# Kernel optimization log

Hardware: AMD Instinct MI355X
Metric: run time of the kernel (lower is better)

The kernel has to match this reference:

```python
import jax, jax.numpy as jnp
import numpy as np

N = 50000      # nodes
E = 1_600_000  # edges per relation
D = 128        # input feature dim
H = 64         # gnn_hidden_channel
R = 3          # hetero relations
NEG_SLOPE = 0.2


def setup_inputs() -> dict:
    key = jax.random.key(0)
    ks = jax.random.split(key, 9)
    x = jax.random.normal(ks[0], (N, D), jnp.float32)
    edge_index = jax.random.randint(ks[1], (R, 2, E), 0, N, dtype=jnp.int32)
    edge_weight = jax.random.uniform(ks[2], (R, E), jnp.float32)
    W0 = jax.random.normal(ks[3], (R, D, H), jnp.float32) / np.float32(np.sqrt(D))
    W1 = jax.random.normal(ks[4], (R, H, H), jnp.float32) / np.float32(np.sqrt(H))
    W2 = jax.random.normal(ks[5], (R, H, H), jnp.float32) / np.float32(np.sqrt(H))
    a_src = jax.random.normal(ks[6], (R, 3, H), jnp.float32) * 0.1
    a_dst = jax.random.normal(ks[7], (R, 3, H), jnp.float32) * 0.1
    bias = jnp.zeros((R, 3, H), jnp.float32)
    return {"x": x, "edge_weight": edge_weight, "W0": W0, "W1": W1, "W2": W2,
            "a_src": a_src, "a_dst": a_dst, "bias": bias, "edge_index": edge_index}


def gat_layer(x, src, dst, ew, W, a_s, a_d, b):
    # GATConv, heads=1: h = xW; e = LeakyReLU(a_s.h_src + a_d.h_dst); softmax over dst
    h = x @ W                                  # [N, H]
    alpha_s = h @ a_s                          # [N]
    alpha_d = h @ a_d                          # [N]
    e = jax.nn.leaky_relu(alpha_s[src] + alpha_d[dst], NEG_SLOPE)  # [Etot]
    m = jax.ops.segment_max(e, dst, num_segments=N)                # per-dst max
    e = jnp.exp(e - m[dst])
    s = jax.ops.segment_sum(e, dst, num_segments=N)
    alpha = (e / (s[dst] + 1e-16)) * ew        # edge_weight scales attention
    out = jax.ops.segment_sum(alpha[:, None] * h[src], dst, num_segments=N)
    return out + b


def reference(x, edge_weight, W0, W1, W2, a_src, a_dst, bias, edge_index):
    loop = jnp.arange(N, dtype=edge_index.dtype)   # self-loops (PyG default)
    ones_w = jnp.ones((N,), x.dtype)
    outs = []
    for r in range(R):
        src = jnp.concatenate([edge_index[r, 0], loop])
        dst = jnp.concatenate([edge_index[r, 1], loop])
        ew = jnp.concatenate([edge_weight[r], ones_w])
        Ws = (W0[r], W1[r], W2[r])
        h = x
        for i in range(3):
            h = gat_layer(h, src, dst, ew, Ws[i], a_src[r, i], a_dst[r, i], bias[r, i])
            if i != 2:
                h = jax.nn.relu(h)
        outs.append(h)
    return jnp.concatenate(outs, axis=1)  # [N, R*H] = [N, 192]
```

## Files before the change

kernel.cpp:

```cpp
#include <hip/hip_runtime.h>
#include <math.h>

#define N_NODES 50000
#define E_EDGES 1600000
#define D_IN 128
#define H_DIM 64
#define R_REL 3
#define ETOT (E_EDGES + N_NODES)
#define NEG_SLOPE 0.2f

#define BSHIFT 8
#define BSIZE 256
#define NBUCK ((N_NODES + BSIZE - 1) / BSIZE)
#define CHUNK 4096
#define NBLK ((ETOT + CHUNK - 1) / CHUNK)

template <int DIN>
__global__ __launch_bounds__(256) void gemm_alpha_kernel(
    const float* __restrict__ xin,
    const float* __restrict__ W,
    const float* __restrict__ a_s,
    const float* __restrict__ a_d,
    float* __restrict__ h,
    float* __restrict__ as_out,
    float* __restrict__ ad_out)
{
    constexpr int KC = 64;
    constexpr int XSTR = KC + 4;
    __shared__ __align__(16) float xls[64 * XSTR];
    __shared__ __align__(16) float wls[KC * 64];
    int t = threadIdx.x;
    int n0 = blockIdx.x * 64;
    int nrows = N_NODES - n0; if (nrows > 64) nrows = 64;
    int tn = t >> 4;
    int tc = t & 15;

    float4 acc[4] = {{0,0,0,0},{0,0,0,0},{0,0,0,0},{0,0,0,0}};

    for (int kc = 0; kc < DIN; kc += KC) {
        if (kc) __syncthreads();
        int nf4 = nrows * (KC / 4);
        for (int f = t; f < nf4; f += 256) {
            int row = f >> 4;
            int q = f & 15;
            float4 xv = *reinterpret_cast<const float4*>(
                xin + (size_t)(n0 + row) * DIN + kc + q * 4);
            *reinterpret_cast<float4*>(&xls[row * XSTR + q * 4]) = xv;
        }
        for (int f = t; f < KC * 16; f += 256) {
            int kk = f >> 4;
            int q = f & 15;
            *reinterpret_cast<float4*>(&wls[kk * 64 + q * 4]) =
                *reinterpret_cast<const float4*>(W + (size_t)(kc + kk) * 64 + q * 4);
        }
        __syncthreads();

#pragma unroll
        for (int k4 = 0; k4 < KC / 4; ++k4) {
            float4 av[4], bv[4];
#pragma unroll
            for (int i = 0; i < 4; ++i)
                av[i] = *reinterpret_cast<const float4*>(
                    &xls[(tn * 4 + i) * XSTR + k4 * 4]);
#pragma unroll
            for (int u = 0; u < 4; ++u)
                bv[u] = *reinterpret_cast<const float4*>(
                    &wls[(k4 * 4 + u) * 64 + tc * 4]);
#pragma unroll
            for (int i = 0; i < 4; ++i) {
                acc[i].x = fmaf(av[i].x, bv[0].x, acc[i].x);
                acc[i].y = fmaf(av[i].x, bv[0].y, acc[i].y);
                acc[i].z = fmaf(av[i].x, bv[0].z, acc[i].z);
                acc[i].w = fmaf(av[i].x, bv[0].w, acc[i].w);
                acc[i].x = fmaf(av[i].y, bv[1].x, acc[i].x);
                acc[i].y = fmaf(av[i].y, bv[1].y, acc[i].y);
                acc[i].z = fmaf(av[i].y, bv[1].z, acc[i].z);
                acc[i].w = fmaf(av[i].y, bv[1].w, acc[i].w);
                acc[i].x = fmaf(av[i].z, bv[2].x, acc[i].x);
                acc[i].y = fmaf(av[i].z, bv[2].y, acc[i].y);
                acc[i].z = fmaf(av[i].z, bv[2].z, acc[i].z);
                acc[i].w = fmaf(av[i].z, bv[2].w, acc[i].w);
                acc[i].x = fmaf(av[i].w, bv[3].x, acc[i].x);
                acc[i].y = fmaf(av[i].w, bv[3].y, acc[i].y);
                acc[i].z = fmaf(av[i].w, bv[3].z, acc[i].z);
                acc[i].w = fmaf(av[i].w, bv[3].w, acc[i].w);
            }
        }
    }

    float4 asj = *reinterpret_cast<const float4*>(a_s + tc * 4);
    float4 adj = *reinterpret_cast<const float4*>(a_d + tc * 4);
#pragma unroll
    for (int i = 0; i < 4; ++i) {
        int node = n0 + tn * 4 + i;
        bool ok = node < N_NODES;
        if (ok)
            *reinterpret_cast<float4*>(h + (size_t)node * 64 + tc * 4) = acc[i];
        float vs = acc[i].x * asj.x + acc[i].y * asj.y +
                   acc[i].z * asj.z + acc[i].w * asj.w;
        float vd = acc[i].x * adj.x + acc[i].y * adj.y +
                   acc[i].z * adj.z + acc[i].w * adj.w;
#pragma unroll
        for (int m = 8; m >= 1; m >>= 1) {
            vs += __shfl_xor(vs, m, 64);
            vd += __shfl_xor(vd, m, 64);
        }
        if (ok && tc == 0) {
            as_out[node] = vs;
            ad_out[node] = vd;
        }
    }
}

__global__ __launch_bounds__(256) void partA_hist(const int* __restrict__ dstE,
                                                  int* __restrict__ bh)
{
    __shared__ int hist[NBUCK];
    int t = threadIdx.x, blk = blockIdx.x;
    for (int b = t; b < NBUCK; b += 256) hist[b] = 0;
    __syncthreads();
    int base = blk * CHUNK;
#pragma unroll
    for (int u = 0; u < CHUNK / 256; ++u) {
        int i = base + u * 256 + t;
        if (i < ETOT) {
            int d = (i < E_EDGES) ? dstE[i] : (i - E_EDGES);
            atomicAdd(&hist[d >> BSHIFT], 1);
        }
    }
    __syncthreads();
    for (int b = t; b < NBUCK; b += 256) bh[(size_t)blk * NBUCK + b] = hist[b];
}

__global__ __launch_bounds__(256) void partA2_scan(int* __restrict__ bh,
                                                   int* __restrict__ btot)
{
    __shared__ int tmp[256];
    __shared__ int carry_s;
    int b = blockIdx.x, t = threadIdx.x;
    if (t == 0) carry_s = 0;
    __syncthreads();
    for (int base = 0; base < NBLK; base += 256) {
        int idx = base + t;
        int v = (idx < NBLK) ? bh[(size_t)idx * NBUCK + b] : 0;
        int x = v;
#pragma unroll
        for (int off = 1; off < 256; off <<= 1) {
            tmp[t] = x;
            __syncthreads();
            int a = (t >= off) ? tmp[t - off] : 0;
            __syncthreads();
            x += a;
        }
        int carry = carry_s;
        if (idx < NBLK) bh[(size_t)idx * NBUCK + b] = carry + x - v;
        __syncthreads();
        if (t == 255) carry_s = carry + x;
        __syncthreads();
    }
    if (t == 0) btot[b] = carry_s;
}

__global__ __launch_bounds__(256) void partA3_scan(const int* __restrict__ btot,
                                                   int* __restrict__ bbase)
{
    __shared__ int tmp[256];
    int t = threadIdx.x;
    int v = (t < NBUCK) ? btot[t] : 0;
    int x = v;
#pragma unroll
    for (int off = 1; off < 256; off <<= 1) {
        tmp[t] = x;
        __syncthreads();
        int a = (t >= off) ? tmp[t - off] : 0;
        __syncthreads();
        x += a;
    }
    if (t < NBUCK) bbase[t] = x - v;
    if (t == 255) bbase[NBUCK] = x;
}

__global__ __launch_bounds__(256) void partB_scatter(
    const int* __restrict__ srcE, const int* __restrict__ dstE,
    const float* __restrict__ ewr, const int* __restrict__ bh,
    const int* __restrict__ bbase, int2* __restrict__ psw)
{
    __shared__ int cur[NBUCK];
    int t = threadIdx.x, blk = blockIdx.x;
    for (int b = t; b < NBUCK; b += 256)
        cur[b] = bbase[b] + bh[(size_t)blk * NBUCK + b];
    __syncthreads();
    int base = blk * CHUNK;
#pragma unroll
    for (int u = 0; u < CHUNK / 256; ++u) {
        int i = base + u * 256 + t;
        if (i < ETOT) {
            int s, d;
            float w;
            if (i < E_EDGES) {
                s = srcE[i]; d = dstE[i]; w = ewr[i];
            } else {
                s = d = i - E_EDGES; w = 1.0f;
            }
            int pos = atomicAdd(&cur[d >> BSHIFT], 1);
            int2 pay;
            pay.x = s | ((d & (BSIZE - 1)) << 16);
            pay.y = __float_as_int(w);
            psw[pos] = pay;
        }
    }
}

__global__ __launch_bounds__(256) void partC_sort(
    const int* __restrict__ bbase, const int2* __restrict__ psw,
    int* __restrict__ rs, int2* __restrict__ sedge)
{
    __shared__ int cnt[BSIZE];
    __shared__ int rsl[BSIZE];
    __shared__ int tmp[BSIZE];
    __shared__ int cur[BSIZE];
    int b = blockIdx.x, t = threadIdx.x;
    int lo = b * BSIZE;
    int nn = N_NODES - lo; if (nn > BSIZE) nn = BSIZE;
    int seg0 = bbase[b], seg1 = bbase[b + 1];
    cnt[t] = 0; cur[t] = 0;
    __syncthreads();
    for (int k = seg0 + t; k < seg1; k += 256)
        atomicAdd(&cnt[(psw[k].x >> 16) & 255], 1);
    __syncthreads();
    int v = cnt[t], x = v;
#pragma unroll
    for (int off = 1; off < 256; off <<= 1) {
        tmp[t] = x;
        __syncthreads();
        int a = (t >= off) ? tmp[t - off] : 0;
        __syncthreads();
        x += a;
    }
    rsl[t] = x - v;
    __syncthreads();
    if (t < nn) rs[lo + t] = seg0 + rsl[t];
    if (b == NBUCK - 1 && t == 0) rs[N_NODES] = seg1;
    for (int k = seg0 + t; k < seg1; k += 256) {
        int2 pw = psw[k];
        int dlo = (pw.x >> 16) & 255;
        int pos = seg0 + rsl[dlo] + atomicAdd(&cur[dlo], 1);
        int2 rec;
        rec.x = pw.x & 0xFFFF;
        rec.y = pw.y;
        sedge[pos] = rec;
    }
}

__global__ __launch_bounds__(256) void agg_kernel(
    const int* __restrict__ rs, const int2* __restrict__ sedge,
    const float* __restrict__ as_v, const float* __restrict__ ad_v,
    const float* __restrict__ h,
    const float* __restrict__ bias,
    float* __restrict__ out, int out_stride, int do_relu)
{
    int wave = (int)(((size_t)blockIdx.x * blockDim.x + threadIdx.x) >> 6);
    int lane = threadIdx.x & 63;
    if (wave >= N_NODES) return;
    int beg = rs[wave], end = rs[wave + 1];
    float ad_n = ad_v[wave];

    int sub = lane >> 4;
    int f = lane & 15;
    const float* hf = h + f * 4;

    float ssum = 0.f;
    float4 a0 = {0.f, 0.f, 0.f, 0.f};
    float4 a1 = a0, a2 = a0, a3 = a0;

    for (int cbeg = beg; cbeg < end; cbeg += 64) {
        int rem = end - cbeg;
        int srcv = 0;
        float pq = 0.f;
        if (lane < rem) {
            int2 pe = sedge[cbeg + lane];
            srcv = pe.x;
            float e = as_v[srcv] + ad_n;
            e = (e > 0.f) ? e : NEG_SLOPE * e;
            float p = __expf(e);
            ssum += p;
            pq = p * __int_as_float(pe.y);
        }
        for (int t0 = 0; t0 < rem; t0 += 16) {
            int s0 = __shfl(srcv, t0 + sub, 64);
            float q0 = __shfl(pq, t0 + sub, 64);
            int s1 = __shfl(srcv, t0 + 4 + sub, 64);
            float q1 = __shfl(pq, t0 + 4 + sub, 64);
            int s2 = __shfl(srcv, t0 + 8 + sub, 64);
            float q2 = __shfl(pq, t0 + 8 + sub, 64);
            int s3 = __shfl(srcv, t0 + 12 + sub, 64);
            float q3 = __shfl(pq, t0 + 12 + sub, 64);
            float4 h0 = *reinterpret_cast<const float4*>(hf + (size_t)s0 * 64);
            float4 h1 = *reinterpret_cast<const float4*>(hf + (size_t)s1 * 64);
            float4 h2 = *reinterpret_cast<const float4*>(hf + (size_t)s2 * 64);
            float4 h3 = *reinterpret_cast<const float4*>(hf + (size_t)s3 * 64);
            a0.x = fmaf(q0, h0.x, a0.x);
            a0.y = fmaf(q0, h0.y, a0.y);
            a0.z = fmaf(q0, h0.z, a0.z);
            a0.w = fmaf(q0, h0.w, a0.w);
            a1.x = fmaf(q1, h1.x, a1.x);
            a1.y = fmaf(q1, h1.y, a1.y);
            a1.z = fmaf(q1, h1.z, a1.z);
            a1.w = fmaf(q1, h1.w, a1.w);
            a2.x = fmaf(q2, h2.x, a2.x);
            a2.y = fmaf(q2, h2.y, a2.y);
            a2.z = fmaf(q2, h2.z, a2.z);
            a2.w = fmaf(q2, h2.w, a2.w);
            a3.x = fmaf(q3, h3.x, a3.x);
            a3.y = fmaf(q3, h3.y, a3.y);
            a3.z = fmaf(q3, h3.z, a3.z);
            a3.w = fmaf(q3, h3.w, a3.w);
        }
    }

    float4 acc;
    acc.x = (a0.x + a1.x) + (a2.x + a3.x);
    acc.y = (a0.y + a1.y) + (a2.y + a3.y);
    acc.z = (a0.z + a1.z) + (a2.z + a3.z);
    acc.w = (a0.w + a1.w) + (a2.w + a3.w);

#pragma unroll
    for (int off = 32; off > 0; off >>= 1) ssum += __shfl_xor(ssum, off, 64);
    acc.x += __shfl_xor(acc.x, 16, 64);
    acc.y += __shfl_xor(acc.y, 16, 64);
    acc.z += __shfl_xor(acc.z, 16, 64);
    acc.w += __shfl_xor(acc.w, 16, 64);
    acc.x += __shfl_xor(acc.x, 32, 64);
    acc.y += __shfl_xor(acc.y, 32, 64);
    acc.z += __shfl_xor(acc.z, 32, 64);
    acc.w += __shfl_xor(acc.w, 32, 64);

    if (sub == 0) {
        float inv = 1.f / (ssum + 1e-16f);
        const float4 bv = *reinterpret_cast<const float4*>(bias + f * 4);
        float4 o;
        o.x = fmaf(acc.x, inv, bv.x);
        o.y = fmaf(acc.y, inv, bv.y);
        o.z = fmaf(acc.z, inv, bv.z);
        o.w = fmaf(acc.w, inv, bv.w);
        if (do_relu) {
            o.x = fmaxf(o.x, 0.f);
            o.y = fmaxf(o.y, 0.f);
            o.z = fmaxf(o.z, 0.f);
            o.w = fmaxf(o.w, 0.f);
        }
        *reinterpret_cast<float4*>(out + (size_t)wave * out_stride + f * 4) = o;
    }
}

extern "C" void kernel_launch(void* const* d_in, const int* in_sizes, int n_in,
                              void* d_out, int out_size, void* d_ws, size_t ws_size,
                              hipStream_t stream)
{
    (void)in_sizes; (void)n_in; (void)out_size; (void)ws_size;
    const float* x = (const float*)d_in[0];
    const float* edge_weight = (const float*)d_in[1];
    const float* W0 = (const float*)d_in[2];
    const float* W1 = (const float*)d_in[3];
    const float* W2 = (const float*)d_in[4];
    const float* a_src = (const float*)d_in[5];
    const float* a_dst = (const float*)d_in[6];
    const float* bias = (const float*)d_in[7];
    const int* edge_index = (const int*)d_in[8];
    float* out = (float*)d_out;

    char* ws = (char*)d_ws;
    size_t off = 0;
    auto alloc = [&](size_t bytes) {
        void* p = ws + off;
        off += (bytes + 255) & ~(size_t)255;
        return p;
    };
    int2* sedge = (int2*)alloc((size_t)ETOT * 8);
    int2* psw = (int2*)alloc((size_t)ETOT * 8);
    int* bh = (int*)alloc((size_t)NBLK * NBUCK * 4);
    int* btot = (int*)alloc((size_t)NBUCK * 4);
    int* bbase = (int*)alloc((size_t)(NBUCK + 1) * 4);
    int* rs = (int*)alloc((size_t)(N_NODES + 1) * 4);
    float* hbuf = (float*)alloc((size_t)N_NODES * 64 * 4);
    float* xbuf = (float*)alloc((size_t)N_NODES * 64 * 4);
    float* asv = (float*)alloc((size_t)N_NODES * 4);
    float* adv = (float*)alloc((size_t)N_NODES * 4);

    const int WAVE_BLOCKS = (N_NODES * 64 + 255) / 256;
    const int GEMM_BLOCKS = (N_NODES + 63) / 64;

    for (int r = 0; r < R_REL; ++r) {
        const int* srcE = edge_index + (size_t)r * 2 * E_EDGES;
        const int* dstE = srcE + E_EDGES;
        const float* ewr = edge_weight + (size_t)r * E_EDGES;

        partA_hist<<<NBLK, 256, 0, stream>>>(dstE, bh);
        partA2_scan<<<NBUCK, 256, 0, stream>>>(bh, btot);
        partA3_scan<<<1, 256, 0, stream>>>(btot, bbase);
        partB_scatter<<<NBLK, 256, 0, stream>>>(srcE, dstE, ewr, bh, bbase, psw);
        partC_sort<<<NBUCK, 256, 0, stream>>>(bbase, psw, rs, sedge);

        for (int i = 0; i < 3; ++i) {
            const float* Wl = (i == 0) ? (W0 + (size_t)r * D_IN * H_DIM)
                            : (i == 1) ? (W1 + (size_t)r * H_DIM * H_DIM)
                                       : (W2 + (size_t)r * H_DIM * H_DIM);
            const float* asr = a_src + ((size_t)r * 3 + i) * H_DIM;
            const float* adr = a_dst + ((size_t)r * 3 + i) * H_DIM;
            const float* br = bias + ((size_t)r * 3 + i) * H_DIM;

            if (i == 0)
                gemm_alpha_kernel<D_IN><<<GEMM_BLOCKS, 256, 0, stream>>>(
                    x, Wl, asr, adr, hbuf, asv, adv);
            else
                gemm_alpha_kernel<H_DIM><<<GEMM_BLOCKS, 256, 0, stream>>>(
                    xbuf, Wl, asr, adr, hbuf, asv, adv);

            if (i < 2)
                agg_kernel<<<WAVE_BLOCKS, 256, 0, stream>>>(
                    rs, sedge, asv, adv, hbuf, br, xbuf, 64, 1);
            else
                agg_kernel<<<WAVE_BLOCKS, 256, 0, stream>>>(
                    rs, sedge, asv, adv, hbuf, br, out + r * 64, 192, 0);
        }
    }
}
```

Before: 856.2 us.

## Batch CSR build across relations, sort buckets in place, pipeline aggregation gathers

The histogram, scan, scatter and bucket-sort kernels now run once for all three relations, with the relation index taken from the block index. This cuts launch count and gives each launch a larger grid. Buckets shrink to 128 nodes and chunks grow to 8192 edges, so the block-level scan becomes a single pass. The bucket sort stages each bucket in LDS and writes back in place, which removes the psw buffer. The aggregation loop now prefetches the next group of neighbour rows before doing the FMAs on the current group, and clamps each chunk to 64 lanes. The in-place sort falls back to global reads for buckets larger than CCAP, which would race with its own writes if a bucket ever overflowed.

```diff
diff --git a/kernel.cpp b/kernel.cpp
--- a/kernel.cpp
+++ b/kernel.cpp
@@ -9,11 +9,12 @@
 #define ETOT (E_EDGES + N_NODES)
 #define NEG_SLOPE 0.2f
 
-#define BSHIFT 8
-#define BSIZE 256
+#define BSHIFT 7
+#define BSIZE 128
 #define NBUCK ((N_NODES + BSIZE - 1) / BSIZE)
-#define CHUNK 4096
+#define CHUNK 8192
 #define NBLK ((ETOT + CHUNK - 1) / CHUNK)
+#define CCAP 5120
 
 template <int DIN>
 __global__ __launch_bounds__(256) void gemm_alpha_kernel(
@@ -112,15 +113,18 @@
     }
 }
 
-__global__ __launch_bounds__(256) void partA_hist(const int* __restrict__ dstE,
+__global__ __launch_bounds__(256) void partA_hist(const int* __restrict__ edge_index,
                                                   int* __restrict__ bh)
 {
     __shared__ int hist[NBUCK];
-    int t = threadIdx.x, blk = blockIdx.x;
+    int t = threadIdx.x;
+    int r = blockIdx.x / NBLK;
+    int blk = blockIdx.x % NBLK;
+    const int* dstE = edge_index + (size_t)r * 2 * E_EDGES + E_EDGES;
     for (int b = t; b < NBUCK; b += 256) hist[b] = 0;
     __syncthreads();
     int base = blk * CHUNK;
-#pragma unroll
+#pragma unroll 4
     for (int u = 0; u < CHUNK / 256; ++u) {
         int i = base + u * 256 + t;
         if (i < ETOT) {
@@ -129,20 +133,46 @@
         }
     }
     __syncthreads();
-    for (int b = t; b < NBUCK; b += 256) bh[(size_t)blk * NBUCK + b] = hist[b];
+    int* bh_r = bh + (size_t)r * NBLK * NBUCK;
+    for (int b = t; b < NBUCK; b += 256) bh_r[(size_t)blk * NBUCK + b] = hist[b];
 }
 
 __global__ __launch_bounds__(256) void partA2_scan(int* __restrict__ bh,
                                                    int* __restrict__ btot)
 {
     __shared__ int tmp[256];
+    int r = blockIdx.x / NBUCK;
+    int b = blockIdx.x % NBUCK;
+    int t = threadIdx.x;
+    int* bh_r = bh + (size_t)r * NBLK * NBUCK;
+    int v = (t < NBLK) ? bh_r[(size_t)t * NBUCK + b] : 0;
+    int x = v;
+#pragma unroll
+    for (int off = 1; off < 256; off <<= 1) {
+        tmp[t] = x;
+        __syncthreads();
+        int a = (t >= off) ? tmp[t - off] : 0;
+        __syncthreads();
+        x += a;
+    }
+    if (t < NBLK) bh_r[(size_t)t * NBUCK + b] = x - v;
+    if (t == 255) btot[r * NBUCK + b] = x;
+}
+
+__global__ __launch_bounds__(256) void partA3_scan(const int* __restrict__ btot,
+                                                   int* __restrict__ bbase)
+{
+    __shared__ int tmp[256];
     __shared__ int carry_s;
-    int b = blockIdx.x, t = threadIdx.x;
+    int r = blockIdx.x;
+    int t = threadIdx.x;
+    const int* row = btot + r * NBUCK;
+    int* outb = bbase + r * (NBUCK + 1);
     if (t == 0) carry_s = 0;
     __syncthreads();
-    for (int base = 0; base < NBLK; base += 256) {
+    for (int base = 0; base < NBUCK; base += 256) {
         int idx = base + t;
-        int v = (idx < NBLK) ? bh[(size_t)idx * NBUCK + b] : 0;
+        int v = (idx < NBUCK) ? row[idx] : 0;
         int x = v;
 #pragma unroll
         for (int off = 1; off < 256; off <<= 1) {
@@ -153,45 +183,34 @@
             x += a;
         }
         int carry = carry_s;
-        if (idx < NBLK) bh[(size_t)idx * NBUCK + b] = carry + x - v;
+        if (idx < NBUCK) outb[idx] = carry + x - v;
         __syncthreads();
         if (t == 255) carry_s = carry + x;
         __syncthreads();
     }
-    if (t == 0) btot[b] = carry_s;
-}
-
-__global__ __launch_bounds__(256) void partA3_scan(const int* __restrict__ btot,
-                                                   int* __restrict__ bbase)
-{
-    __shared__ int tmp[256];
-    int t = threadIdx.x;
-    int v = (t < NBUCK) ? btot[t] : 0;
-    int x = v;
-#pragma unroll
-    for (int off = 1; off < 256; off <<= 1) {
-        tmp[t] = x;
-        __syncthreads();
-        int a = (t >= off) ? tmp[t - off] : 0;
-        __syncthreads();
-        x += a;
-    }
-    if (t < NBUCK) bbase[t] = x - v;
-    if (t == 255) bbase[NBUCK] = x;
+    if (t == 0) outb[NBUCK] = carry_s;
 }
 
 __global__ __launch_bounds__(256) void partB_scatter(
-    const int* __restrict__ srcE, const int* __restrict__ dstE,
-    const float* __restrict__ ewr, const int* __restrict__ bh,
-    const int* __restrict__ bbase, int2* __restrict__ psw)
+    const int* __restrict__ edge_index, const float* __restrict__ edge_weight,
+    const int* __restrict__ bh, const int* __restrict__ bbase,
+    int2* __restrict__ sedge)
 {
     __shared__ int cur[NBUCK];
-    int t = threadIdx.x, blk = blockIdx.x;
+    int t = threadIdx.x;
+    int r = blockIdx.x / NBLK;
+    int blk = blockIdx.x % NBLK;
+    const int* srcE = edge_index + (size_t)r * 2 * E_EDGES;
+    const int* dstE = srcE + E_EDGES;
+    const float* ewr = edge_weight + (size_t)r * E_EDGES;
+    const int* bh_r = bh + (size_t)r * NBLK * NBUCK;
+    const int* bbase_r = bbase + r * (NBUCK + 1);
+    int2* se_r = sedge + (size_t)r * ETOT;
     for (int b = t; b < NBUCK; b += 256)
-        cur[b] = bbase[b] + bh[(size_t)blk * NBUCK + b];
+        cur[b] = bbase_r[b] + bh_r[(size_t)blk * NBUCK + b];
     __syncthreads();
     int base = blk * CHUNK;
-#pragma unroll
+#pragma unroll 4
     for (int u = 0; u < CHUNK / 256; ++u) {
         int i = base + u * 256 + t;
         if (i < ETOT) {
@@ -206,49 +225,60 @@
             int2 pay;
             pay.x = s | ((d & (BSIZE - 1)) << 16);
             pay.y = __float_as_int(w);
-            psw[pos] = pay;
+            se_r[pos] = pay;
         }
     }
 }
 
 __global__ __launch_bounds__(256) void partC_sort(
-    const int* __restrict__ bbase, const int2* __restrict__ psw,
-    int* __restrict__ rs, int2* __restrict__ sedge)
-{
+    const int* __restrict__ bbase, int2* __restrict__ sedge,
+    int* __restrict__ rs)
+{
+    __shared__ int2 stage[CCAP];
     __shared__ int cnt[BSIZE];
     __shared__ int rsl[BSIZE];
     __shared__ int tmp[BSIZE];
     __shared__ int cur[BSIZE];
-    int b = blockIdx.x, t = threadIdx.x;
+    int r = blockIdx.x / NBUCK;
+    int b = blockIdx.x % NBUCK;
+    int t = threadIdx.x;
+    const int* bbase_r = bbase + r * (NBUCK + 1);
+    int* rs_r = rs + r * (N_NODES + 1);
+    int2* se_r = sedge + (size_t)r * ETOT;
     int lo = b * BSIZE;
     int nn = N_NODES - lo; if (nn > BSIZE) nn = BSIZE;
-    int seg0 = bbase[b], seg1 = bbase[b + 1];
-    cnt[t] = 0; cur[t] = 0;
-    __syncthreads();
-    for (int k = seg0 + t; k < seg1; k += 256)
-        atomicAdd(&cnt[(psw[k].x >> 16) & 255], 1);
-    __syncthreads();
-    int v = cnt[t], x = v;
-#pragma unroll
-    for (int off = 1; off < 256; off <<= 1) {
-        tmp[t] = x;
-        __syncthreads();
-        int a = (t >= off) ? tmp[t - off] : 0;
+    int seg0 = bbase_r[b], seg1 = bbase_r[b + 1];
+    int len = seg1 - seg0;
+    if (t < BSIZE) { cnt[t] = 0; cur[t] = 0; }
+    __syncthreads();
+    for (int k = t; k < len; k += 256) {
+        int2 pw = se_r[seg0 + k];
+        if (k < CCAP) stage[k] = pw;
+        atomicAdd(&cnt[(pw.x >> 16) & (BSIZE - 1)], 1);
+    }
+    __syncthreads();
+    int v = 0, x = 0;
+    if (t < BSIZE) { v = cnt[t]; x = v; }
+#pragma unroll
+    for (int off = 1; off < BSIZE; off <<= 1) {
+        if (t < BSIZE) tmp[t] = x;
+        __syncthreads();
+        int a = (t < BSIZE && t >= off) ? tmp[t - off] : 0;
         __syncthreads();
         x += a;
     }
-    rsl[t] = x - v;
-    __syncthreads();
-    if (t < nn) rs[lo + t] = seg0 + rsl[t];
-    if (b == NBUCK - 1 && t == 0) rs[N_NODES] = seg1;
-    for (int k = seg0 + t; k < seg1; k += 256) {
-        int2 pw = psw[k];
-        int dlo = (pw.x >> 16) & 255;
-        int pos = seg0 + rsl[dlo] + atomicAdd(&cur[dlo], 1);
+    if (t < BSIZE) rsl[t] = x - v;
+    __syncthreads();
+    if (t < nn) rs_r[lo + t] = seg0 + rsl[t];
+    if (b == NBUCK - 1 && t == 0) rs_r[N_NODES] = seg1;
+    for (int k = t; k < len; k += 256) {
+        int2 pw = (k < CCAP) ? stage[k] : se_r[seg0 + k];
+        int dlo = (pw.x >> 16) & (BSIZE - 1);
+        int pos = rsl[dlo] + atomicAdd(&cur[dlo], 1);
         int2 rec;
         rec.x = pw.x & 0xFFFF;
         rec.y = pw.y;
-        sedge[pos] = rec;
+        se_r[seg0 + pos] = rec;
     }
 }
 
@@ -275,6 +305,7 @@
 
     for (int cbeg = beg; cbeg < end; cbeg += 64) {
         int rem = end - cbeg;
+        if (rem > 64) rem = 64;
         int srcv = 0;
         float pq = 0.f;
         if (lane < rem) {
@@ -286,19 +317,31 @@
             ssum += p;
             pq = p * __int_as_float(pe.y);
         }
-        for (int t0 = 0; t0 < rem; t0 += 16) {
-            int s0 = __shfl(srcv, t0 + sub, 64);
-            float q0 = __shfl(pq, t0 + sub, 64);
-            int s1 = __shfl(srcv, t0 + 4 + sub, 64);
-            float q1 = __shfl(pq, t0 + 4 + sub, 64);
-            int s2 = __shfl(srcv, t0 + 8 + sub, 64);
-            float q2 = __shfl(pq, t0 + 8 + sub, 64);
-            int s3 = __shfl(srcv, t0 + 12 + sub, 64);
-            float q3 = __shfl(pq, t0 + 12 + sub, 64);
-            float4 h0 = *reinterpret_cast<const float4*>(hf + (size_t)s0 * 64);
-            float4 h1 = *reinterpret_cast<const float4*>(hf + (size_t)s1 * 64);
-            float4 h2 = *reinterpret_cast<const float4*>(hf + (size_t)s2 * 64);
-            float4 h3 = *reinterpret_cast<const float4*>(hf + (size_t)s3 * 64);
+        int s0 = __shfl(srcv, sub, 64);
+        float q0 = __shfl(pq, sub, 64);
+        int s1 = __shfl(srcv, 4 + sub, 64);
+        float q1 = __shfl(pq, 4 + sub, 64);
+        int s2 = __shfl(srcv, 8 + sub, 64);
+        float q2 = __shfl(pq, 8 + sub, 64);
+        int s3 = __shfl(srcv, 12 + sub, 64);
+        float q3 = __shfl(pq, 12 + sub, 64);
+        float4 h0 = *reinterpret_cast<const float4*>(hf + (size_t)s0 * 64);
+        float4 h1 = *reinterpret_cast<const float4*>(hf + (size_t)s1 * 64);
+        float4 h2 = *reinterpret_cast<const float4*>(hf + (size_t)s2 * 64);
+        float4 h3 = *reinterpret_cast<const float4*>(hf + (size_t)s3 * 64);
+        for (int t0 = 16; t0 < rem; t0 += 16) {
+            int ns0 = __shfl(srcv, t0 + sub, 64);
+            float nq0 = __shfl(pq, t0 + sub, 64);
+            int ns1 = __shfl(srcv, t0 + 4 + sub, 64);
+            float nq1 = __shfl(pq, t0 + 4 + sub, 64);
+            int ns2 = __shfl(srcv, t0 + 8 + sub, 64);
+            float nq2 = __shfl(pq, t0 + 8 + sub, 64);
+            int ns3 = __shfl(srcv, t0 + 12 + sub, 64);
+            float nq3 = __shfl(pq, t0 + 12 + sub, 64);
+            float4 nh0 = *reinterpret_cast<const float4*>(hf + (size_t)ns0 * 64);
+            float4 nh1 = *reinterpret_cast<const float4*>(hf + (size_t)ns1 * 64);
+            float4 nh2 = *reinterpret_cast<const float4*>(hf + (size_t)ns2 * 64);
+            float4 nh3 = *reinterpret_cast<const float4*>(hf + (size_t)ns3 * 64);
             a0.x = fmaf(q0, h0.x, a0.x);
             a0.y = fmaf(q0, h0.y, a0.y);
             a0.z = fmaf(q0, h0.z, a0.z);
@@ -315,7 +358,27 @@
             a3.y = fmaf(q3, h3.y, a3.y);
             a3.z = fmaf(q3, h3.z, a3.z);
             a3.w = fmaf(q3, h3.w, a3.w);
-        }
+            q0 = nq0; h0 = nh0;
+            q1 = nq1; h1 = nh1;
+            q2 = nq2; h2 = nh2;
+            q3 = nq3; h3 = nh3;
+        }
+        a0.x = fmaf(q0, h0.x, a0.x);
+        a0.y = fmaf(q0, h0.y, a0.y);
+        a0.z = fmaf(q0, h0.z, a0.z);
+        a0.w = fmaf(q0, h0.w, a0.w);
+        a1.x = fmaf(q1, h1.x, a1.x);
+        a1.y = fmaf(q1, h1.y, a1.y);
+        a1.z = fmaf(q1, h1.z, a1.z);
+        a1.w = fmaf(q1, h1.w, a1.w);
+        a2.x = fmaf(q2, h2.x, a2.x);
+        a2.y = fmaf(q2, h2.y, a2.y);
+        a2.z = fmaf(q2, h2.z, a2.z);
+        a2.w = fmaf(q2, h2.w, a2.w);
+        a3.x = fmaf(q3, h3.x, a3.x);
+        a3.y = fmaf(q3, h3.y, a3.y);
+        a3.z = fmaf(q3, h3.z, a3.z);
+        a3.w = fmaf(q3, h3.w, a3.w);
     }
 
     float4 acc;
@@ -376,12 +439,11 @@
         off += (bytes + 255) & ~(size_t)255;
         return p;
     };
-    int2* sedge = (int2*)alloc((size_t)ETOT * 8);
-    int2* psw = (int2*)alloc((size_t)ETOT * 8);
-    int* bh = (int*)alloc((size_t)NBLK * NBUCK * 4);
-    int* btot = (int*)alloc((size_t)NBUCK * 4);
-    int* bbase = (int*)alloc((size_t)(NBUCK + 1) * 4);
-    int* rs = (int*)alloc((size_t)(N_NODES + 1) * 4);
+    int2* sedge = (int2*)alloc((size_t)R_REL * ETOT * 8);
+    int* bh = (int*)alloc((size_t)R_REL * NBLK * NBUCK * 4);
+    int* btot = (int*)alloc((size_t)R_REL * NBUCK * 4);
+    int* bbase = (int*)alloc((size_t)R_REL * (NBUCK + 1) * 4);
+    int* rs = (int*)alloc((size_t)R_REL * (N_NODES + 1) * 4);
     float* hbuf = (float*)alloc((size_t)N_NODES * 64 * 4);
     float* xbuf = (float*)alloc((size_t)N_NODES * 64 * 4);
     float* asv = (float*)alloc((size_t)N_NODES * 4);
@@ -390,16 +452,15 @@
     const int WAVE_BLOCKS = (N_NODES * 64 + 255) / 256;
     const int GEMM_BLOCKS = (N_NODES + 63) / 64;
 
+    partA_hist<<<R_REL * NBLK, 256, 0, stream>>>(edge_index, bh);
+    partA2_scan<<<R_REL * NBUCK, 256, 0, stream>>>(bh, btot);
+    partA3_scan<<<R_REL, 256, 0, stream>>>(btot, bbase);
+    partB_scatter<<<R_REL * NBLK, 256, 0, stream>>>(edge_index, edge_weight, bh, bbase, sedge);
+    partC_sort<<<R_REL * NBUCK, 256, 0, stream>>>(bbase, sedge, rs);
+
     for (int r = 0; r < R_REL; ++r) {
-        const int* srcE = edge_index + (size_t)r * 2 * E_EDGES;
-        const int* dstE = srcE + E_EDGES;
-        const float* ewr = edge_weight + (size_t)r * E_EDGES;
-
-        partA_hist<<<NBLK, 256, 0, stream>>>(dstE, bh);
-        partA2_scan<<<NBUCK, 256, 0, stream>>>(bh, btot);
-        partA3_scan<<<1, 256, 0, stream>>>(btot, bbase);
-        partB_scatter<<<NBLK, 256, 0, stream>>>(srcE, dstE, ewr, bh, bbase, psw);
-        partC_sort<<<NBUCK, 256, 0, stream>>>(bbase, psw, rs, sedge);
+        const int* rs_r = rs + r * (N_NODES + 1);
+        const int2* se_r = sedge + (size_t)r * ETOT;
 
         for (int i = 0; i < 3; ++i) {
             const float* Wl = (i == 0) ? (W0 + (size_t)r * D_IN * H_DIM)
@@ -418,10 +479,10 @@
 
             if (i < 2)
                 agg_kernel<<<WAVE_BLOCKS, 256, 0, stream>>>(
-                    rs, sedge, asv, adv, hbuf, br, xbuf, 64, 1);
+                    rs_r, se_r, asv, adv, hbuf, br, xbuf, 64, 1);
             else
                 agg_kernel<<<WAVE_BLOCKS, 256, 0, stream>>>(
-                    rs, sedge, asv, adv, hbuf, br, out + r * 64, 192, 0);
-        }
-    }
-}
+                    rs_r, se_r, asv, adv, hbuf, br, out + r * 64, 192, 0);
+        }
+    }
+}
```

After: 833.3 us. -2.7%, faster.
